# Kernel optimization log

Measured on AMD Instinct MI355X. Metric: run time of the kernel, lower is better.

## Reference

```python
import jax, jax.numpy as jnp
import numpy as np

N, E, B = 50000, 800000, 256
NODE_DIM, EDGE_DIM, H = 4, 1, 64


def setup_inputs() -> dict:
    key = jax.random.key(0)
    ks = jax.random.split(key, 32)
    def rn(k, shape, scale=0.1):
        return (jax.random.normal(k, shape) * scale).astype(jnp.float32)
    inp = {
        "x": jax.random.normal(ks[0], (N, NODE_DIM), dtype=jnp.float32),
        "edge_index": jax.random.randint(ks[1], (2, E), 0, N, dtype=jnp.int32),
        "edge_attr": jax.random.normal(ks[2], (E, EDGE_DIM), dtype=jnp.float32),
        "batch": jnp.sort(jax.random.randint(ks[3], (N,), 0, B, dtype=jnp.int32)),
        # embed Linear(node_dim -> H); weights stored [in, out]
        "embed_W": rn(ks[4], (NODE_DIM, H)), "embed_b": jnp.zeros((H,), jnp.float32),
        # GATv2 conv1
        "c1_Wl": rn(ks[5], (H, H)), "c1_bl": jnp.zeros((H,), jnp.float32),
        "c1_Wr": rn(ks[6], (H, H)), "c1_br": jnp.zeros((H,), jnp.float32),
        "c1_We": rn(ks[7], (EDGE_DIM, H)),
        "c1_att": rn(ks[8], (H,)), "c1_bias": jnp.zeros((H,), jnp.float32),
        # GATv2 conv2
        "c2_Wl": rn(ks[9], (H, H)), "c2_bl": jnp.zeros((H,), jnp.float32),
        "c2_Wr": rn(ks[10], (H, H)), "c2_br": jnp.zeros((H,), jnp.float32),
        "c2_We": rn(ks[11], (EDGE_DIM, H)),
        "c2_att": rn(ks[12], (H,)), "c2_bias": jnp.zeros((H,), jnp.float32),
        # ODE func: Linear(H, 2H) -> tanh -> Linear(2H, H)
        "ode_W1": rn(ks[13], (H, 2 * H)), "ode_b1": jnp.zeros((2 * H,), jnp.float32),
        "ode_W2": rn(ks[14], (2 * H, H)), "ode_b2": jnp.zeros((H,), jnp.float32),
        # predictor: Linear(2H, 32) -> SiLU -> (Dropout eval=id) -> Linear(32, 1)
        "pred_W1": rn(ks[15], (2 * H, 32)), "pred_b1": jnp.zeros((32,), jnp.float32),
        "pred_W2": rn(ks[16], (32, 1)), "pred_b2": jnp.zeros((1,), jnp.float32),
    }
    return inp


def gatv2_conv(x, src, dst, edge_attr, Wl, bl, Wr, br, We, att, bias):
    # PyG GATv2Conv, heads=1: xl feeds messages (source), xr the target side.
    xl = x @ Wl + bl                       # [N,H]
    xr = x @ Wr + br                       # [N,H]
    m = xl[src] + xr[dst] + edge_attr @ We  # [E,H]
    m = jnp.where(m > 0, m, 0.2 * m)        # leaky_relu(0.2)
    e = m @ att                             # [E]
    emax = jax.ops.segment_max(e, dst, num_segments=N)
    ex = jnp.exp(e - emax[dst])
    denom = jax.ops.segment_sum(ex, dst, num_segments=N)
    alpha = ex / denom[dst]                 # softmax over incoming edges
    out = jax.ops.segment_sum(alpha[:, None] * xl[src], dst, num_segments=N)
    return out + bias


def reference(x, edge_index, edge_attr, batch,
              embed_W, embed_b,
              c1_Wl, c1_bl, c1_Wr, c1_br, c1_We, c1_att, c1_bias,
              c2_Wl, c2_bl, c2_Wr, c2_br, c2_We, c2_att, c2_bias,
              ode_W1, ode_b1, ode_W2, ode_b2,
              pred_W1, pred_b1, pred_W2, pred_b2):
    src, dst = edge_index[0], edge_index[1]
    silu = jax.nn.silu
    h = x @ embed_W + embed_b
    h = silu(gatv2_conv(h, src, dst, edge_attr, c1_Wl, c1_bl, c1_Wr, c1_br, c1_We, c1_att, c1_bias))
    h = silu(gatv2_conv(h, src, dst, edge_attr, c2_Wl, c2_bl, c2_Wr, c2_br, c2_We, c2_att, c2_bias))

    # one fixed-grid RK4 step from t=0 to t=1 (torchdiffeq rk4 on t=[0,1])
    def f(y):
        return jnp.tanh(y @ ode_W1 + ode_b1) @ ode_W2 + ode_b2
    k1 = f(h)
    k2 = f(h + 0.5 * k1)
    k3 = f(h + 0.5 * k2)
    k4 = f(h + k3)
    h = h + (k1 + 2.0 * k2 + 2.0 * k3 + k4) / 6.0

    # global mean / max pool over graphs
    counts = jax.ops.segment_sum(jnp.ones((N,), h.dtype), batch, num_segments=B)
    gmean = jax.ops.segment_sum(h, batch, num_segments=B) / jnp.maximum(counts, 1.0)[:, None]
    gmax = jax.ops.segment_max(h, batch, num_segments=B)
    gmax = jnp.where(counts[:, None] > 0, gmax, 0.0)
    g = jnp.concatenate([gmean, gmax], axis=1)  # [B, 2H]

    out = silu(g @ pred_W1 + pred_b1) @ pred_W2 + pred_b2  # dropout in eval = identity
    return out[:, 0]
```

## Files before the change

kernel.cpp:

```cpp
#include <hip/hip_runtime.h>
#include <math.h>

#define Nn 50000
#define Ee 800000
#define Bb 256
#define Hh 64
#define TPB 256
#define CHUNK 512

__global__ void k_embed(const float* __restrict__ x, const float* __restrict__ W,
                        const float* __restrict__ b, float* __restrict__ h) {
    int idx = blockIdx.x * blockDim.x + threadIdx.x;
    if (idx >= Nn * Hh) return;
    int n = idx >> 6, j = idx & 63;
    float acc = b[j];
#pragma unroll
    for (int d = 0; d < 4; ++d) acc += x[n * 4 + d] * W[d * Hh + j];
    h[idx] = acc;
}

__global__ void k_hist(const int* __restrict__ dst, int* __restrict__ counts) {
    int e = blockIdx.x * blockDim.x + threadIdx.x;
    if (e < Ee) atomicAdd(&counts[dst[e]], 1);
}

__global__ void k_scan1(const int* __restrict__ counts, int* __restrict__ off,
                        int* __restrict__ chunksum) {
    __shared__ int s[CHUNK];
    int t = threadIdx.x;
    int base = blockIdx.x * CHUNK;
    int v = (base + t < Nn) ? counts[base + t] : 0;
    s[t] = v;
    __syncthreads();
    for (int d = 1; d < CHUNK; d <<= 1) {
        int u = (t >= d) ? s[t - d] : 0;
        __syncthreads();
        s[t] += u;
        __syncthreads();
    }
    if (base + t < Nn) off[base + t + 1] = s[t];
    if (t == CHUNK - 1) chunksum[blockIdx.x] = s[t];
}

__global__ void k_scan2(int* __restrict__ chunksum, int nch) {
    if (blockIdx.x == 0 && threadIdx.x == 0) {
        int run = 0;
        for (int i = 0; i < nch; ++i) { int v = chunksum[i]; chunksum[i] = run; run += v; }
    }
}

__global__ void k_scan3(int* __restrict__ off, const int* __restrict__ chunkoff,
                        int* __restrict__ cursor) {
    int i = blockIdx.x * blockDim.x + threadIdx.x;
    if (i > Nn) return;
    int v;
    if (i == 0) { off[0] = 0; v = 0; }
    else {
        v = off[i] + chunkoff[(i - 1) >> 9];
        off[i] = v;
    }
    if (i < Nn) cursor[i] = v;
}

__global__ void k_scatter(const int* __restrict__ src, const int* __restrict__ dst,
                          const float* __restrict__ ea, int* __restrict__ cursor,
                          int2* __restrict__ epack) {
    int e = blockIdx.x * blockDim.x + threadIdx.x;
    if (e >= Ee) return;
    int d = dst[e];
    int p = atomicAdd(&cursor[d], 1);
    epack[p] = make_int2(src[e], __float_as_int(ea[e]));
}

__global__ __launch_bounds__(256) void k_lin(const float* __restrict__ h,
                      const float* __restrict__ Wl, const float* __restrict__ bl,
                      const float* __restrict__ Wr, const float* __restrict__ br,
                      float* __restrict__ xl, float* __restrict__ xr) {
    int lane = threadIdx.x & 63, w = threadIdx.x >> 6;
    int n0 = blockIdx.x * 16 + w * 4;
    float al[4], ar[4];
#pragma unroll
    for (int q = 0; q < 4; ++q) { al[q] = bl[lane]; ar[q] = br[lane]; }
    for (int i4 = 0; i4 < 16; ++i4) {
        float4 hv[4];
#pragma unroll
        for (int q = 0; q < 4; ++q)
            hv[q] = *(const float4*)(h + (n0 + q) * 64 + i4 * 4);
#pragma unroll
        for (int u = 0; u < 4; ++u) {
            int i = i4 * 4 + u;
            float wlv = Wl[i * 64 + lane];
            float wrv = Wr[i * 64 + lane];
#pragma unroll
            for (int q = 0; q < 4; ++q) {
                float hq = ((const float*)&hv[q])[u];
                al[q] += hq * wlv;
                ar[q] += hq * wrv;
            }
        }
    }
#pragma unroll
    for (int q = 0; q < 4; ++q) {
        xl[(n0 + q) * 64 + lane] = al[q];
        xr[(n0 + q) * 64 + lane] = ar[q];
    }
}

__global__ void k_conv(const float* __restrict__ xl, const float* __restrict__ xr,
                       const int2* __restrict__ epack, const int* __restrict__ off,
                       const float* __restrict__ We, const float* __restrict__ att,
                       const float* __restrict__ bias, float* __restrict__ hout) {
    int gid = blockIdx.x * blockDim.x + threadIdx.x;
    int n = gid >> 6, lane = gid & 63;
    if (n >= Nn) return;
    int g = lane >> 4, l16 = lane & 15;
    int s = off[n], t = off[n + 1];
    float4 xr4 = *(const float4*)(xr + (size_t)n * 64 + l16 * 4);
    float4 We4 = *(const float4*)(We + l16 * 4);
    float4 at4 = *(const float4*)(att + l16 * 4);
    float4 acc = make_float4(0.f, 0.f, 0.f, 0.f);
    float m_run = -1e30f, s_run = 0.f;
    for (int c = s; c < t; c += 4) {
        int e = c + g;
        bool valid = e < t;
        int2 pk = valid ? epack[e] : epack[c];
        int sr = pk.x;
        float ceav = valid ? __int_as_float(pk.y) : 0.f;
        float4 row = *(const float4*)(xl + (size_t)sr * 64 + l16 * 4);
        float mx_ = row.x + xr4.x + ceav * We4.x;
        float my_ = row.y + xr4.y + ceav * We4.y;
        float mz_ = row.z + xr4.z + ceav * We4.z;
        float mw_ = row.w + xr4.w + ceav * We4.w;
        mx_ = mx_ > 0.f ? mx_ : 0.2f * mx_;
        my_ = my_ > 0.f ? my_ : 0.2f * my_;
        mz_ = mz_ > 0.f ? mz_ : 0.2f * mz_;
        mw_ = mw_ > 0.f ? mw_ : 0.2f * mw_;
        float pv = mx_ * at4.x + my_ * at4.y + mz_ * at4.z + mw_ * at4.w;
#pragma unroll
        for (int o = 1; o < 16; o <<= 1) pv += __shfl_xor(pv, o);
        float ee = valid ? pv : -1e30f;
        float cm = ee;
        cm = fmaxf(cm, __shfl_xor(cm, 16));
        cm = fmaxf(cm, __shfl_xor(cm, 32));
        float m_new = fmaxf(m_run, cm);
        float f = __expf(m_run - m_new);
        acc.x *= f; acc.y *= f; acc.z *= f; acc.w *= f; s_run *= f;
        float w = __expf(ee - m_new);
        acc.x += w * row.x; acc.y += w * row.y;
        acc.z += w * row.z; acc.w += w * row.w;
        s_run += w;
        m_run = m_new;
    }
#pragma unroll
    for (int o = 16; o <= 32; o <<= 1) {
        acc.x += __shfl_xor(acc.x, o); acc.y += __shfl_xor(acc.y, o);
        acc.z += __shfl_xor(acc.z, o); acc.w += __shfl_xor(acc.w, o);
        s_run += __shfl_xor(s_run, o);
    }
    float4 b4 = *(const float4*)(bias + l16 * 4);
    float inv = (t > s) ? 1.f / s_run : 0.f;
    float4 o4;
    o4.x = acc.x * inv + b4.x; o4.y = acc.y * inv + b4.y;
    o4.z = acc.z * inv + b4.z; o4.w = acc.w * inv + b4.w;
    o4.x = o4.x / (1.f + __expf(-o4.x));
    o4.y = o4.y / (1.f + __expf(-o4.y));
    o4.z = o4.z / (1.f + __expf(-o4.z));
    o4.w = o4.w / (1.f + __expf(-o4.w));
    if (lane < 16) *(float4*)(hout + (size_t)n * 64 + l16 * 4) = o4;
}

template <int STAGE>
__global__ __launch_bounds__(128) void k_ode(float* __restrict__ h,
        const float* __restrict__ kprev,
        const float* __restrict__ W1, const float* __restrict__ b1,
        const float* __restrict__ W2, const float* __restrict__ b2,
        float* __restrict__ kout, float* __restrict__ ksum) {
    __shared__ float yt[16][64];
    __shared__ float zt[16][128];
    int t = threadIdx.x;
    int nb = blockIdx.x * 16;
    {
        const float cf = (STAGE == 3) ? 1.0f : 0.5f;
#pragma unroll
        for (int r = 0; r < 2; ++r) {
            int f = t + r * 128;
            int nn = f >> 4, jj = (f & 15) * 4;
            float4 hv = *(const float4*)(h + (size_t)(nb + nn) * 64 + jj);
            if (STAGE != 0) {
                float4 kv = *(const float4*)(kprev + (size_t)(nb + nn) * 64 + jj);
                hv.x += cf * kv.x; hv.y += cf * kv.y; hv.z += cf * kv.z; hv.w += cf * kv.w;
            }
            *(float4*)&yt[nn][jj] = hv;
        }
    }
    __syncthreads();
    {
        int k = t;
        float acc1[16];
#pragma unroll
        for (int q = 0; q < 16; ++q) acc1[q] = b1[k];
        for (int i4 = 0; i4 < 16; ++i4) {
            float wv4[4];
#pragma unroll
            for (int u = 0; u < 4; ++u) wv4[u] = W1[(i4 * 4 + u) * 128 + k];
#pragma unroll
            for (int half = 0; half < 2; ++half) {
                float4 yv[8];
#pragma unroll
                for (int q8 = 0; q8 < 8; ++q8)
                    yv[q8] = *(const float4*)&yt[half * 8 + q8][i4 * 4];
#pragma unroll
                for (int u = 0; u < 4; ++u)
#pragma unroll
                    for (int q8 = 0; q8 < 8; ++q8)
                        acc1[half * 8 + q8] += ((const float*)&yv[q8])[u] * wv4[u];
            }
        }
#pragma unroll
        for (int q = 0; q < 16; ++q) zt[q][k] = tanhf(acc1[q]);
    }
    __syncthreads();
    {
        int j = t & 63, wg = t >> 6;
        float acc2[8];
#pragma unroll
        for (int q = 0; q < 8; ++q) acc2[q] = b2[j];
        for (int k4 = 0; k4 < 32; ++k4) {
            float wv2[4];
#pragma unroll
            for (int u = 0; u < 4; ++u) wv2[u] = W2[(k4 * 4 + u) * 64 + j];
            float4 zv[8];
#pragma unroll
            for (int q = 0; q < 8; ++q)
                zv[q] = *(const float4*)&zt[wg * 8 + q][k4 * 4];
#pragma unroll
            for (int u = 0; u < 4; ++u)
#pragma unroll
                for (int q = 0; q < 8; ++q)
                    acc2[q] += ((const float*)&zv[q])[u] * wv2[u];
        }
#pragma unroll
        for (int q = 0; q < 8; ++q) {
            size_t gi = (size_t)(nb + wg * 8 + q) * 64 + j;
            if (STAGE == 0)      { kout[gi] = acc2[q]; ksum[gi] = acc2[q]; }
            else if (STAGE == 3) { h[gi] = h[gi] + (ksum[gi] + acc2[q]) * (1.f / 6.f); }
            else                 { kout[gi] = acc2[q]; ksum[gi] += 2.f * acc2[q]; }
        }
    }
}

__global__ void k_binit(int* __restrict__ gs, int* __restrict__ ge) {
    int b = threadIdx.x;
    if (b < Bb) { gs[b] = 0; ge[b] = 0; }
}

__global__ void k_bounds(const int* __restrict__ batch, int* __restrict__ gs,
                         int* __restrict__ ge) {
    int n = blockIdx.x * blockDim.x + threadIdx.x;
    if (n >= Nn) return;
    int b = batch[n];
    if (n == 0 || batch[n - 1] != b) gs[b] = n;
    if (n == Nn - 1 || batch[n + 1] != b) ge[b] = n + 1;
}

__global__ void k_pool(const float* __restrict__ h, const int* __restrict__ gs,
                       const int* __restrict__ ge, float* __restrict__ g) {
    int b = blockIdx.x;
    int s = gs[b], e = ge[b];
    int w = threadIdx.x >> 6, lane = threadIdx.x & 63;
    float sum = 0.f, mx = -1e30f;
    for (int n = s + w; n < e; n += 4) {
        float v = h[n * Hh + lane];
        sum += v;
        mx = fmaxf(mx, v);
    }
    __shared__ float ssum[4][64], smx[4][64];
    ssum[w][lane] = sum;
    smx[w][lane] = mx;
    __syncthreads();
    if (threadIdx.x < 64) {
        int j = threadIdx.x;
        float su = ssum[0][j] + ssum[1][j] + ssum[2][j] + ssum[3][j];
        float m2 = fmaxf(fmaxf(smx[0][j], smx[1][j]), fmaxf(smx[2][j], smx[3][j]));
        int cnt = e - s;
        g[b * 2 * Hh + j] = (cnt > 0) ? su / (float)cnt : 0.f;
        g[b * 2 * Hh + Hh + j] = (cnt > 0) ? m2 : 0.f;
    }
}

__global__ void k_pred(const float* __restrict__ g, const float* __restrict__ W1,
                       const float* __restrict__ b1, const float* __restrict__ W2,
                       const float* __restrict__ b2, float* __restrict__ out) {
    int gid = blockIdx.x * blockDim.x + threadIdx.x;
    int b = gid >> 6, lane = gid & 63;
    if (b >= Bb) return;
    int hh = lane & 31, half = lane >> 5;
    const float* gr = g + b * 2 * Hh + half * Hh;
    float a = 0.f;
#pragma unroll 8
    for (int i = 0; i < Hh; ++i) a += gr[i] * W1[(half * Hh + i) * 32 + hh];
    a += __shfl_xor(a, 32);
    a += b1[hh];
    float sl = a / (1.f + expf(-a));
    float partial = (half == 0) ? sl * W2[hh] : 0.f;
#pragma unroll
    for (int o = 32; o > 0; o >>= 1) partial += __shfl_xor(partial, o);
    if (lane == 0) out[b] = partial + b2[0];
}

extern "C" void kernel_launch(void* const* d_in, const int* in_sizes, int n_in,
                              void* d_out, int out_size, void* d_ws, size_t ws_size,
                              hipStream_t stream) {
    const float* x     = (const float*)d_in[0];
    const int*   ei    = (const int*)d_in[1];
    const float* ea    = (const float*)d_in[2];
    const int*   batch = (const int*)d_in[3];
    const float* embW  = (const float*)d_in[4];
    const float* embB  = (const float*)d_in[5];
    const float* c1Wl = (const float*)d_in[6];  const float* c1bl = (const float*)d_in[7];
    const float* c1Wr = (const float*)d_in[8];  const float* c1br = (const float*)d_in[9];
    const float* c1We = (const float*)d_in[10]; const float* c1att = (const float*)d_in[11];
    const float* c1bias = (const float*)d_in[12];
    const float* c2Wl = (const float*)d_in[13]; const float* c2bl = (const float*)d_in[14];
    const float* c2Wr = (const float*)d_in[15]; const float* c2br = (const float*)d_in[16];
    const float* c2We = (const float*)d_in[17]; const float* c2att = (const float*)d_in[18];
    const float* c2bias = (const float*)d_in[19];
    const float* oW1 = (const float*)d_in[20]; const float* ob1 = (const float*)d_in[21];
    const float* oW2 = (const float*)d_in[22]; const float* ob2 = (const float*)d_in[23];
    const float* pW1 = (const float*)d_in[24]; const float* pb1 = (const float*)d_in[25];
    const float* pW2 = (const float*)d_in[26]; const float* pb2 = (const float*)d_in[27];
    float* out = (float*)d_out;

    float* fws = (float*)d_ws;
    size_t NH = (size_t)Nn * Hh;
    float* h    = fws;
    float* xl   = fws + NH;
    float* xr   = fws + 2 * NH;
    float* ksum = fws + 3 * NH;
    int2*  epack = (int2*)(fws + 4 * NH);
    float* g    = (float*)(epack + Ee);
    int* iws = (int*)(g + (size_t)Bb * 128);
    int* counts = iws;
    int* off    = counts + Nn;
    int* cursor = off + Nn + 1;
    int* chk    = cursor + Nn;
    int* gs     = chk + 128;
    int* ge     = gs + Bb;

    const int* src = ei;
    const int* dst = ei + Ee;

    hipMemsetAsync(counts, 0, Nn * sizeof(int), stream);
    k_embed<<<(Nn * Hh + TPB - 1) / TPB, TPB, 0, stream>>>(x, embW, embB, h);
    k_hist<<<(Ee + TPB - 1) / TPB, TPB, 0, stream>>>(dst, counts);
    k_scan1<<<(Nn + CHUNK - 1) / CHUNK, CHUNK, 0, stream>>>(counts, off, chk);
    k_scan2<<<1, 64, 0, stream>>>(chk, (Nn + CHUNK - 1) / CHUNK);
    k_scan3<<<(Nn + 1 + TPB - 1) / TPB, TPB, 0, stream>>>(off, chk, cursor);
    k_scatter<<<(Ee + TPB - 1) / TPB, TPB, 0, stream>>>(src, dst, ea, cursor, epack);

    k_lin<<<Nn / 16, TPB, 0, stream>>>(h, c1Wl, c1bl, c1Wr, c1br, xl, xr);
    k_conv<<<(Nn * 64 + TPB - 1) / TPB, TPB, 0, stream>>>(xl, xr, epack, off, c1We, c1att, c1bias, h);

    k_lin<<<Nn / 16, TPB, 0, stream>>>(h, c2Wl, c2bl, c2Wr, c2br, xl, xr);
    k_conv<<<(Nn * 64 + TPB - 1) / TPB, TPB, 0, stream>>>(xl, xr, epack, off, c2We, c2att, c2bias, h);

    int gOde = Nn / 16;
    k_ode<0><<<gOde, 128, 0, stream>>>(h, h,  oW1, ob1, oW2, ob2, xl, ksum);
    k_ode<1><<<gOde, 128, 0, stream>>>(h, xl, oW1, ob1, oW2, ob2, xr, ksum);
    k_ode<2><<<gOde, 128, 0, stream>>>(h, xr, oW1, ob1, oW2, ob2, xl, ksum);
    k_ode<3><<<gOde, 128, 0, stream>>>(h, xl, oW1, ob1, oW2, ob2, xr, ksum);

    k_binit<<<1, Bb, 0, stream>>>(gs, ge);
    k_bounds<<<(Nn + TPB - 1) / TPB, TPB, 0, stream>>>(batch, gs, ge);
    k_pool<<<Bb, 256, 0, stream>>>(h, gs, ge, g);
    k_pred<<<(Bb * 64 + TPB - 1) / TPB, TPB, 0, stream>>>(g, pW1, pb1, pW2, pb2, out);
}
```

Before: 588.7 us.

## Fuse four RK4 stage kernels into one kernel keeping state on-chip

Replaces the four per-stage ODE launches with a single kernel that runs all RK4 stages for a 16-node tile, holding the base state and weighted k-sum in registers and the stage input in shared memory. This removes the global round trips for the kprev, kout and ksum arrays and three kernel launches. The ksum workspace buffer is dropped. Register pressure rises because h0 and ksum arrays live across the unrolled stage loop, and the extra syncs could hurt occupancy.

```diff
diff --git a/kernel.cpp b/kernel.cpp
--- a/kernel.cpp
+++ b/kernel.cpp
@@ -169,84 +169,86 @@
     if (lane < 16) *(float4*)(hout + (size_t)n * 64 + l16 * 4) = o4;
 }
 
-template <int STAGE>
-__global__ __launch_bounds__(128) void k_ode(float* __restrict__ h,
-        const float* __restrict__ kprev,
+__global__ __launch_bounds__(128) void k_ode4(float* __restrict__ h,
         const float* __restrict__ W1, const float* __restrict__ b1,
-        const float* __restrict__ W2, const float* __restrict__ b2,
-        float* __restrict__ kout, float* __restrict__ ksum) {
+        const float* __restrict__ W2, const float* __restrict__ b2) {
     __shared__ float yt[16][64];
     __shared__ float zt[16][128];
     int t = threadIdx.x;
     int nb = blockIdx.x * 16;
-    {
-        const float cf = (STAGE == 3) ? 1.0f : 0.5f;
-#pragma unroll
-        for (int r = 0; r < 2; ++r) {
-            int f = t + r * 128;
-            int nn = f >> 4, jj = (f & 15) * 4;
-            float4 hv = *(const float4*)(h + (size_t)(nb + nn) * 64 + jj);
-            if (STAGE != 0) {
-                float4 kv = *(const float4*)(kprev + (size_t)(nb + nn) * 64 + jj);
-                hv.x += cf * kv.x; hv.y += cf * kv.y; hv.z += cf * kv.z; hv.w += cf * kv.w;
+    int j = t & 63, wg = t >> 6;
+#pragma unroll
+    for (int r = 0; r < 2; ++r) {
+        int f = t + r * 128;
+        int nn = f >> 4, jj = (f & 15) * 4;
+        *(float4*)&yt[nn][jj] = *(const float4*)(h + (size_t)(nb + nn) * 64 + jj);
+    }
+    float h0[8], ksum[8];
+#pragma unroll
+    for (int q = 0; q < 8; ++q) {
+        h0[q] = h[(size_t)(nb + wg * 8 + q) * 64 + j];
+        ksum[q] = 0.f;
+    }
+    __syncthreads();
+#pragma unroll
+    for (int s = 0; s < 4; ++s) {
+        const float wgt = (s == 1 || s == 2) ? 2.f : 1.f;
+        const float cf = (s == 2) ? 1.f : 0.5f;
+        {
+            int k = t;
+            float acc1[16];
+#pragma unroll
+            for (int q = 0; q < 16; ++q) acc1[q] = b1[k];
+            for (int i4 = 0; i4 < 16; ++i4) {
+                float wv4[4];
+#pragma unroll
+                for (int u = 0; u < 4; ++u) wv4[u] = W1[(i4 * 4 + u) * 128 + k];
+#pragma unroll
+                for (int half = 0; half < 2; ++half) {
+                    float4 yv[8];
+#pragma unroll
+                    for (int q8 = 0; q8 < 8; ++q8)
+                        yv[q8] = *(const float4*)&yt[half * 8 + q8][i4 * 4];
+#pragma unroll
+                    for (int u = 0; u < 4; ++u)
+#pragma unroll
+                        for (int q8 = 0; q8 < 8; ++q8)
+                            acc1[half * 8 + q8] += ((const float*)&yv[q8])[u] * wv4[u];
+                }
             }
-            *(float4*)&yt[nn][jj] = hv;
+#pragma unroll
+            for (int q = 0; q < 16; ++q) zt[q][k] = tanhf(acc1[q]);
         }
-    }
-    __syncthreads();
-    {
-        int k = t;
-        float acc1[16];
-#pragma unroll
-        for (int q = 0; q < 16; ++q) acc1[q] = b1[k];
-        for (int i4 = 0; i4 < 16; ++i4) {
-            float wv4[4];
-#pragma unroll
-            for (int u = 0; u < 4; ++u) wv4[u] = W1[(i4 * 4 + u) * 128 + k];
-#pragma unroll
-            for (int half = 0; half < 2; ++half) {
-                float4 yv[8];
-#pragma unroll
-                for (int q8 = 0; q8 < 8; ++q8)
-                    yv[q8] = *(const float4*)&yt[half * 8 + q8][i4 * 4];
+        __syncthreads();
+        {
+            float acc2[8];
+#pragma unroll
+            for (int q = 0; q < 8; ++q) acc2[q] = b2[j];
+            for (int k4 = 0; k4 < 32; ++k4) {
+                float wv2[4];
+#pragma unroll
+                for (int u = 0; u < 4; ++u) wv2[u] = W2[(k4 * 4 + u) * 64 + j];
+                float4 zv[8];
+#pragma unroll
+                for (int q = 0; q < 8; ++q)
+                    zv[q] = *(const float4*)&zt[wg * 8 + q][k4 * 4];
 #pragma unroll
                 for (int u = 0; u < 4; ++u)
 #pragma unroll
-                    for (int q8 = 0; q8 < 8; ++q8)
-                        acc1[half * 8 + q8] += ((const float*)&yv[q8])[u] * wv4[u];
+                    for (int q = 0; q < 8; ++q)
+                        acc2[q] += ((const float*)&zv[q])[u] * wv2[u];
+            }
+#pragma unroll
+            for (int q = 0; q < 8; ++q) {
+                ksum[q] += wgt * acc2[q];
+                if (s < 3) yt[wg * 8 + q][j] = h0[q] + cf * acc2[q];
             }
         }
-#pragma unroll
-        for (int q = 0; q < 16; ++q) zt[q][k] = tanhf(acc1[q]);
-    }
-    __syncthreads();
-    {
-        int j = t & 63, wg = t >> 6;
-        float acc2[8];
-#pragma unroll
-        for (int q = 0; q < 8; ++q) acc2[q] = b2[j];
-        for (int k4 = 0; k4 < 32; ++k4) {
-            float wv2[4];
-#pragma unroll
-            for (int u = 0; u < 4; ++u) wv2[u] = W2[(k4 * 4 + u) * 64 + j];
-            float4 zv[8];
-#pragma unroll
-            for (int q = 0; q < 8; ++q)
-                zv[q] = *(const float4*)&zt[wg * 8 + q][k4 * 4];
-#pragma unroll
-            for (int u = 0; u < 4; ++u)
-#pragma unroll
-                for (int q = 0; q < 8; ++q)
-                    acc2[q] += ((const float*)&zv[q])[u] * wv2[u];
-        }
-#pragma unroll
-        for (int q = 0; q < 8; ++q) {
-            size_t gi = (size_t)(nb + wg * 8 + q) * 64 + j;
-            if (STAGE == 0)      { kout[gi] = acc2[q]; ksum[gi] = acc2[q]; }
-            else if (STAGE == 3) { h[gi] = h[gi] + (ksum[gi] + acc2[q]) * (1.f / 6.f); }
-            else                 { kout[gi] = acc2[q]; ksum[gi] += 2.f * acc2[q]; }
-        }
-    }
+        __syncthreads();
+    }
+#pragma unroll
+    for (int q = 0; q < 8; ++q)
+        h[(size_t)(nb + wg * 8 + q) * 64 + j] = h0[q] + ksum[q] * (1.f / 6.f);
 }
 
 __global__ void k_binit(int* __restrict__ gs, int* __restrict__ ge) {
@@ -336,8 +338,7 @@
     float* h    = fws;
     float* xl   = fws + NH;
     float* xr   = fws + 2 * NH;
-    float* ksum = fws + 3 * NH;
-    int2*  epack = (int2*)(fws + 4 * NH);
+    int2*  epack = (int2*)(fws + 3 * NH);
     float* g    = (float*)(epack + Ee);
     int* iws = (int*)(g + (size_t)Bb * 128);
     int* counts = iws;
@@ -364,11 +365,7 @@
     k_lin<<<Nn / 16, TPB, 0, stream>>>(h, c2Wl, c2bl, c2Wr, c2br, xl, xr);
     k_conv<<<(Nn * 64 + TPB - 1) / TPB, TPB, 0, stream>>>(xl, xr, epack, off, c2We, c2att, c2bias, h);
 
-    int gOde = Nn / 16;
-    k_ode<0><<<gOde, 128, 0, stream>>>(h, h,  oW1, ob1, oW2, ob2, xl, ksum);
-    k_ode<1><<<gOde, 128, 0, stream>>>(h, xl, oW1, ob1, oW2, ob2, xr, ksum);
-    k_ode<2><<<gOde, 128, 0, stream>>>(h, xr, oW1, ob1, oW2, ob2, xl, ksum);
-    k_ode<3><<<gOde, 128, 0, stream>>>(h, xl, oW1, ob1, oW2, ob2, xr, ksum);
+    k_ode4<<<Nn / 16, 128, 0, stream>>>(h, oW1, ob1, oW2, ob2);
 
     k_binit<<<1, Bb, 0, stream>>>(gs, ge);
     k_bounds<<<(Nn + TPB - 1) / TPB, TPB, 0, stream>>>(batch, gs, ge);
```

Measured after the change: 587.0 us. About the same (-0.3%).
